# Kernel optimization log

Hardware: AMD Instinct MI355X
Metric: run time of the kernel (lower is better)

## Reference

```python
import jax, jax.numpy as jnp
import numpy as np

N = 16384      # nodes per graph (128x128 image)
E = 9 * N      # 8-neighborhood + self edges
C = 512        # input feature channels
M = 32         # matrixSize


def _p(key, shape, scale=0.05):
    return jax.random.normal(key, shape, dtype=jnp.float32) * scale


def setup_inputs() -> dict:
    key = jax.random.key(0)
    ks = jax.random.split(key, 40)
    inp = {
        "cF": jax.random.normal(ks[0], (N, C), dtype=jnp.float32),
        "sF": jax.random.normal(ks[1], (N, C), dtype=jnp.float32),
        "content_edge_index": jax.random.randint(ks[2], (2, E), 0, N),
        "content_selections": jax.random.randint(ks[3], (E,), 0, 9),
        "style_edge_index": jax.random.randint(ks[4], (2, E), 0, N),
        "style_selections": jax.random.randint(ks[5], (E,), 0, 9),
        "compress_W": _p(ks[6], (1, C, M)),   # kernel_size=1 -> 1 selection
        "compress_b": _p(ks[7], (M,)),
        "unzip_W": _p(ks[8], (1, M, C)),
        "unzip_b": _p(ks[9], (C,)),
    }
    i = 10
    for net in ("cnet", "snet"):
        for j, (ci, co) in enumerate([(C, 256), (256, 128), (128, M)], 1):
            inp[f"{net}_W{j}"] = _p(ks[i], (9, ci, co)); i += 1  # kernel_size=3 -> 9 selections
            inp[f"{net}_b{j}"] = _p(ks[i], (co,)); i += 1
        inp[f"{net}_fcW"] = _p(ks[i], (M * M, M * M)); i += 1   # torch Linear [out,in]
        inp[f"{net}_fcb"] = _p(ks[i], (M * M,)); i += 1
    return inp


def sel_conv(x, edge_index, sel, W, b):
    """SelectionConv: per-selection weight, gather from src, scatter-add to dst.
    x: [N,Cin], W: [S,Cin,Cout]. Edges with selection >= S are masked (kernel_size=1)."""
    S = W.shape[0]
    t = jnp.einsum('nc,scd->snd', x, W)              # [S, N, Cout]
    src, dst = edge_index[0], edge_index[1]
    msgs = t[jnp.minimum(sel, S - 1), src]           # [E, Cout]
    msgs = jnp.where((sel < S)[:, None], msgs, 0.0)
    return jax.ops.segment_sum(msgs, dst, num_segments=x.shape[0]) + b


def cnn_net(x, ei, sel, W1, b1, W2, b2, W3, b3, fcW, fcb):
    h = jax.nn.relu(sel_conv(x, ei, sel, W1, b1))
    h = jax.nn.relu(sel_conv(h, ei, sel, W2, b2))
    h = sel_conv(h, ei, sel, W3, b3)                 # [N, M]
    g = (h.T @ h) / h.shape[0]                       # [M, M] gram
    return g.reshape(-1) @ fcW.T + fcb               # [M*M]


def reference(cF, sF, content_edge_index, content_selections, style_edge_index,
              style_selections, compress_W, compress_b, unzip_W, unzip_b,
              cnet_W1, cnet_b1, cnet_W2, cnet_b2, cnet_W3, cnet_b3, cnet_fcW, cnet_fcb,
              snet_W1, snet_b1, snet_W2, snet_b2, snet_W3, snet_b3, snet_fcW, snet_fcb):
    cMean = jnp.mean(cF, axis=0, keepdims=True)
    cFc = cF - cMean
    sMean = jnp.mean(sF, axis=0, keepdims=True)
    sFc = sF - sMean
    compress_content = sel_conv(cFc, content_edge_index, content_selections,
                                compress_W, compress_b)          # [N, M]
    m = compress_W.shape[2]
    cMat = cnn_net(cFc, content_edge_index, content_selections,
                   cnet_W1, cnet_b1, cnet_W2, cnet_b2, cnet_W3, cnet_b3,
                   cnet_fcW, cnet_fcb).reshape(m, m)
    sMat = cnn_net(sFc, style_edge_index, style_selections,
                   snet_W1, snet_b1, snet_W2, snet_b2, snet_W3, snet_b3,
                   snet_fcW, snet_fcb).reshape(m, m)
    transmatrix = sMat @ cMat                                    # [M, M]
    transfeature = (transmatrix @ compress_content.T).T          # [N, M]
    out = sel_conv(transfeature, content_edge_index, content_selections,
                   unzip_W, unzip_b) + sMean                     # [N, 512]
    return (out, transmatrix)
```

## Files before the change

kernel.cpp:

```cpp
#include <hip/hip_runtime.h>
#include <hip/hip_bf16.h>
#include <cstddef>
#include <cstdint>

#define NN 16384
#define EE (9*NN)
#define CC 512

typedef __attribute__((ext_vector_type(4))) float f32x4;
typedef __attribute__((ext_vector_type(8))) short bf16x8;

static inline int idiv(int a, int b){ return (a+b-1)/b; }

__device__ __forceinline__ float bf2f(unsigned short u){
    union{unsigned u; float f;} v; v.u = ((unsigned)u) << 16; return v.f;
}
__device__ __forceinline__ unsigned short f2bf(float f){
    union{float f; unsigned u;} v; v.f = f;
    unsigned r = v.u + 0x7fffu + ((v.u >> 16) & 1u);
    return (unsigned short)(r >> 16);
}

__device__ __forceinline__ void gload16(const void* gsrc, void* ldst){
    __builtin_amdgcn_global_load_lds(
        (const __attribute__((address_space(1))) unsigned int*)gsrc,
        (__attribute__((address_space(3))) unsigned int*)ldst,
        16, 0, 0);
}


__global__ void zero_i(int* __restrict__ p, int n){
    int i = blockIdx.x*256 + threadIdx.x; if (i < n) p[i] = 0;
}

__global__ void colsum2(const float* __restrict__ F0, float* __restrict__ cs0,
                        const float* __restrict__ F1, float* __restrict__ cs1){
    const float* F = blockIdx.z ? F1 : F0;
    float* cs = blockIdx.z ? cs1 : cs0;
    const int RPB = NN/256;
    int r0 = blockIdx.x * RPB;
    int c4 = threadIdx.x;
    float4 s = {0.f,0.f,0.f,0.f};
    for (int r = 0; r < RPB; ++r){
        float4 v = ((const float4*)(F + (size_t)(r0+r)*CC))[c4];
        s.x += v.x; s.y += v.y; s.z += v.z; s.w += v.w;
    }
    atomicAdd(&cs[c4*4+0], s.x);
    atomicAdd(&cs[c4*4+1], s.y);
    atomicAdd(&cs[c4*4+2], s.z);
    atomicAdd(&cs[c4*4+3], s.w);
}

__global__ void center2(const float* __restrict__ F0, const float* __restrict__ cs0,
                        ushort4* __restrict__ o0,
                        const float* __restrict__ F1, const float* __restrict__ cs1,
                        ushort4* __restrict__ o1){
    const float* F = blockIdx.z ? F1 : F0;
    const float* cs = blockIdx.z ? cs1 : cs0;
    ushort4* o = blockIdx.z ? o1 : o0;
    int i = blockIdx.x*256 + threadIdx.x;
    float4 v = ((const float4*)F)[i];
    int c = (i << 2) & (CC-1);
    float4 m = *(const float4*)(cs + c);
    ushort4 r;
    r.x = f2bf(v.x - m.x*(1.f/NN));
    r.y = f2bf(v.y - m.y*(1.f/NN));
    r.z = f2bf(v.z - m.z*(1.f/NN));
    r.w = f2bf(v.w - m.w*(1.f/NN));
    o[i] = r;
}

__global__ void wtrans(const float* __restrict__ W, unsigned short* __restrict__ Wt,
                       int S, int K, int Cout, int Npad, int Kpad){
    int idx = blockIdx.x*256 + threadIdx.x;
    if (idx >= Npad*Kpad) return;
    int colp = idx / Kpad, k = idx - colp*Kpad;
    int s = colp / Cout, j = colp - s*Cout;
    float v = 0.f;
    if (s < S && k < K) v = W[((size_t)s*K + k)*Cout + j];
    Wt[idx] = f2bf(v);
}

__global__ void wtrans2z(const float* __restrict__ W0, const float* __restrict__ W1,
                         unsigned short* __restrict__ Wt0, unsigned short* __restrict__ Wt1,
                         int K, int Cout){
    __shared__ float tile[32][129];
    int s = blockIdx.z % 9;
    const float* W = (blockIdx.z < 9) ? W0 : W1;
    unsigned short* Wt = (blockIdx.z < 9) ? Wt0 : Wt1;
    int jb = blockIdx.x*128, kb = blockIdx.y*32;
    const float* Ws = W + (size_t)s*K*Cout;
    for (int r = 0; r < 32; ++r)
        tile[r][threadIdx.x] = Ws[(size_t)(kb+r)*Cout + jb + threadIdx.x];
    __syncthreads();
    int kk = threadIdx.x & 31, j0 = threadIdx.x >> 5;
    for (int jj = j0; jj < 128; jj += 4)
        Wt[(size_t)(s*Cout + jb + jj)*K + kb + kk] = f2bf(tile[kk][jj]);
}

__global__ void csr_count3(const int* __restrict__ cDst, const int* __restrict__ sDst,
                           const int* __restrict__ cSel,
                           int* __restrict__ cCnt, int* __restrict__ sCnt, int* __restrict__ cCnt0){
    int e = blockIdx.x*256 + threadIdx.x;
    if (e >= EE) return;
    int z = blockIdx.z;
    if (z == 0)      atomicAdd(&cCnt[cDst[e]], 1);
    else if (z == 1) atomicAdd(&sCnt[sDst[e]], 1);
    else if (cSel[e] == 0) atomicAdd(&cCnt0[cDst[e]], 1);
}
__global__ void csr_scan3(const int* __restrict__ c0, const int* __restrict__ c1,
                          const int* __restrict__ c2,
                          int* __restrict__ r0, int* __restrict__ r1, int* __restrict__ r2){
    const int* cnt = blockIdx.z==0 ? c0 : (blockIdx.z==1 ? c1 : c2);
    int* rowptr    = blockIdx.z==0 ? r0 : (blockIdx.z==1 ? r1 : r2);
    __shared__ int part[1024];
    int t = threadIdx.x;
    int base = t*16, s = 0;
    int local[16];
    #pragma unroll
    for (int i = 0; i < 16; ++i){ local[i] = s; s += cnt[base+i]; }
    part[t] = s; __syncthreads();
    for (int off = 1; off < 1024; off <<= 1){
        int v = (t >= off) ? part[t-off] : 0;
        __syncthreads();
        part[t] += v;
        __syncthreads();
    }
    int pre = (t == 0) ? 0 : part[t-1];
    #pragma unroll
    for (int i = 0; i < 16; ++i) rowptr[base+i] = pre + local[i];
    if (t == 1023) rowptr[NN] = part[1023];
}
__global__ void csr_fill3(const int* __restrict__ cSrc, const int* __restrict__ cDst,
                          const int* __restrict__ cSel,
                          const int* __restrict__ sSrc, const int* __restrict__ sDst,
                          const int* __restrict__ sSel,
                          const int* __restrict__ cRow, const int* __restrict__ sRow,
                          const int* __restrict__ cRow0,
                          int* __restrict__ cCur, int* __restrict__ sCur, int* __restrict__ cCur0,
                          int* __restrict__ cEl, int* __restrict__ sEl, int* __restrict__ cEl0){
    int e = blockIdx.x*256 + threadIdx.x;
    if (e >= EE) return;
    int z = blockIdx.z;
    if (z == 0){
        int d = cDst[e];
        int p = atomicAdd(&cCur[d], 1);
        cEl[cRow[d] + p] = (cSrc[e] << 4) | cSel[e];
    } else if (z == 1){
        int d = sDst[e];
        int p = atomicAdd(&sCur[d], 1);
        sEl[sRow[d] + p] = (sSrc[e] << 4) | sSel[e];
    } else if (cSel[e] == 0){
        int d = cDst[e];
        int p = atomicAdd(&cCur0[d], 1);
        cEl0[cRow0[d] + p] = cSrc[e];
    }
}

template<typename OutT>
__global__ __launch_bounds__(256, 2)
void mfma_gemm(const unsigned short* __restrict__ A0, const unsigned short* __restrict__ Bt0,
               OutT* __restrict__ C0,
               const unsigned short* __restrict__ A1, const unsigned short* __restrict__ Bt1,
               OutT* __restrict__ C1, int K, int N){
    const unsigned short* A  = blockIdx.z ? A1 : A0;
    const unsigned short* Bt = blockIdx.z ? Bt1 : Bt0;
    OutT* C = blockIdx.z ? C1 : C0;
    __shared__ __align__(16) unsigned short As[128*64];
    __shared__ __align__(16) unsigned short Bs[128*64];
    const int tid  = threadIdx.x;
    const int wave = tid >> 6, lane = tid & 63;
    const int row0 = blockIdx.y << 7, col0 = blockIdx.x << 7;
    const int wm = wave >> 1, wn = wave & 1;
    const int fr = lane & 15, fq = lane >> 4;
    f32x4 acc[4][4] = {};
    for (int k0 = 0; k0 < K; k0 += 64){
        __syncthreads();
        #pragma unroll
        for (int i = 0; i < 4; ++i){
            int chb = (wave*4 + i) * 64;
            int ch  = chb + lane;
            int r   = ch >> 3, c8 = ch & 7;
            gload16((const char*)(A  + (size_t)(row0 + r)*K + k0) + c8*16, As + chb*8);
            gload16((const char*)(Bt + (size_t)(col0 + r)*K + k0) + c8*16, Bs + chb*8);
        }
        __syncthreads();
        #pragma unroll
        for (int ks = 0; ks < 2; ++ks){
            bf16x8 av[4], bv[4];
            #pragma unroll
            for (int m = 0; m < 4; ++m)
                av[m] = *(const bf16x8*)(As + ((wm<<6)+(m<<4)+fr)*64 + (ks<<5) + (fq<<3));
            #pragma unroll
            for (int n = 0; n < 4; ++n)
                bv[n] = *(const bf16x8*)(Bs + ((wn<<6)+(n<<4)+fr)*64 + (ks<<5) + (fq<<3));
            #pragma unroll
            for (int m = 0; m < 4; ++m)
                #pragma unroll
                for (int n = 0; n < 4; ++n)
                    acc[m][n] = __builtin_amdgcn_mfma_f32_16x16x32_bf16(bv[n], av[m], acc[m][n], 0, 0, 0);
        }
    }
    #pragma unroll
    for (int m = 0; m < 4; ++m){
        int row = row0 + (wm<<6) + (m<<4) + fr;
        OutT* crow = C + (size_t)row*N + col0 + (wn<<6) + (fq<<2);
        #pragma unroll
        for (int n = 0; n < 4; ++n){
            if constexpr (sizeof(OutT) == 2){
                unsigned lo = f2bf(acc[m][n][0]) | ((unsigned)f2bf(acc[m][n][1]) << 16);
                unsigned hi = f2bf(acc[m][n][2]) | ((unsigned)f2bf(acc[m][n][3]) << 16);
                uint2 pk; pk.x = lo; pk.y = hi;
                *(uint2*)((unsigned short*)crow + (n<<4)) = pk;
            } else {
                float4 pk; pk.x = acc[m][n][0]; pk.y = acc[m][n][1];
                pk.z = acc[m][n][2]; pk.w = acc[m][n][3];
                *(float4*)((float*)crow + (n<<4)) = pk;
            }
        }
    }
}

template<int MQ, int NQ>
__device__ __forceinline__ void mfmaq(f32x4 (&acc)[8][4], bf16x8 (&a)[4][2], bf16x8 (&b)[2][2]){
    #pragma unroll
    for (int m = 0; m < 4; ++m)
        #pragma unroll
        for (int n = 0; n < 2; ++n)
            #pragma unroll
            for (int ks = 0; ks < 2; ++ks)
                acc[MQ*4+m][NQ*2+n] = __builtin_amdgcn_mfma_f32_16x16x32_bf16(
                    b[n][ks], a[m][ks], acc[MQ*4+m][NQ*2+n], 0, 0, 0);
}

#define MIDBAR() do{ __builtin_amdgcn_s_barrier(); \
                     asm volatile("s_waitcnt lgkmcnt(0)" ::: "memory"); \
                     __builtin_amdgcn_sched_barrier(0); \
                     __builtin_amdgcn_s_setprio(1); }while(0)
#define ENDBAR() do{ __builtin_amdgcn_s_setprio(0); \
                     __builtin_amdgcn_s_barrier(); }while(0)

template<int NK>
__global__ __launch_bounds__(512, 1)
void gemm8p(const unsigned short* __restrict__ Ain0, const unsigned short* __restrict__ Btin0,
            unsigned short* __restrict__ Cout0,
            const unsigned short* __restrict__ Ain1, const unsigned short* __restrict__ Btin1,
            unsigned short* __restrict__ Cout1, int N){
    constexpr int LDK = NK*64;
    const unsigned short* A  = blockIdx.z ? Ain1 : Ain0;
    const unsigned short* Bt = blockIdx.z ? Btin1 : Btin0;
    unsigned short* C = blockIdx.z ? Cout1 : Cout0;
    __shared__ __align__(16) unsigned short lds[2][4][8192];
    const int tid = threadIdx.x, w = tid >> 6, l = tid & 63;
    const int nbx = gridDim.x;
    const int nwg = gridDim.x * gridDim.y;
    int blin = blockIdx.y * nbx + blockIdx.x;
    int sw = (blin & 7) * (nwg >> 3) + (blin >> 3);
    const int bx = sw % nbx, by = sw / nbx;
    const int row0 = by << 8, col0 = bx << 8;
    const int wm = w >> 2, wn = w & 3;
    const int fr = l & 15, fq = l >> 4;

    f32x4 acc[8][4] = {};
    bf16x8 a[4][2], b01[2][2], b23[2][2];

    const unsigned short* gA = A + (size_t)row0 * LDK;
    const unsigned short* gB = Bt + (size_t)col0 * LDK;

    auto STG = [&](const unsigned short* gbase, int t, int half, unsigned short* ldsHalf){
        #pragma unroll
        for (int s = 0; s < 2; ++s){
            int o = s*8192 + w*1024 + l*16;
            int q = o ^ ((o >> 3) & 0x70);
            int row = q >> 7;
            gload16((const char*)(gbase + (size_t)(half*128 + row)*LDK + t*64) + (q & 127),
                    ldsHalf + s*4096 + w*512);
        }
    };
    auto LDA = [&](const unsigned short* half, int rb, int ks){
        int lg = (rb*16 + fr)*128 + ks*64 + fq*16;
        int ph = lg ^ ((fr & 7) << 4);
        return *(const bf16x8*)((const char*)half + ph);
    };

    STG(gA, 0, 0, &lds[0][0][0]); STG(gA, 0, 1, &lds[0][1][0]);
    STG(gB, 0, 0, &lds[0][2][0]); STG(gB, 0, 1, &lds[0][3][0]);
    STG(gB, 1, 0, &lds[1][2][0]); STG(gB, 1, 1, &lds[1][3][0]);
    asm volatile("s_waitcnt vmcnt(4)" ::: "memory");
    __builtin_amdgcn_s_barrier();

    const unsigned short* myA[2] = { &lds[0][wm][0], &lds[1][wm][0] };
    const unsigned short* myB[2] = { &lds[0][2+(wn>>1)][0], &lds[1][2+(wn>>1)][0] };
    const int brb = (wn & 1) * 4;

    for (int i = 0; i < NK/2; ++i){
        const int t0 = 2*i, t1 = 2*i + 1;
        #pragma unroll
        for (int m = 0; m < 4; ++m){ a[m][0] = LDA(myA[0], m, 0); a[m][1] = LDA(myA[0], m, 1); }
        #pragma unroll
        for (int n = 0; n < 2; ++n){ b01[n][0] = LDA(myB[0], brb+n, 0); b01[n][1] = LDA(myB[0], brb+n, 1); }
        STG(gA, t1, 0, &lds[1][0][0]);
        MIDBAR(); mfmaq<0,0>(acc, a, b01); ENDBAR();
        #pragma unroll
        for (int n = 0; n < 2; ++n){ b23[n][0] = LDA(myB[0], brb+2+n, 0); b23[n][1] = LDA(myB[0], brb+2+n, 1); }
        STG(gA, t1, 1, &lds[1][1][0]);
        MIDBAR(); mfmaq<0,1>(acc, a, b23); ENDBAR();
        #pragma unroll
        for (int m = 0; m < 4; ++m){ a[m][0] = LDA(myA[0], 4+m, 0); a[m][1] = LDA(myA[0], 4+m, 1); }
        STG(gB, t0+2, 0, &lds[0][2][0]);
        MIDBAR(); mfmaq<1,0>(acc, a, b01); ENDBAR();
        STG(gB, t0+2, 1, &lds[0][3][0]);
        asm volatile("s_waitcnt vmcnt(4)" ::: "memory");
        MIDBAR(); mfmaq<1,1>(acc, a, b23); ENDBAR();
        #pragma unroll
        for (int m = 0; m < 4; ++m){ a[m][0] = LDA(myA[1], m, 0); a[m][1] = LDA(myA[1], m, 1); }
        #pragma unroll
        for (int n = 0; n < 2; ++n){ b01[n][0] = LDA(myB[1], brb+n, 0); b01[n][1] = LDA(myB[1], brb+n, 1); }
        STG(gA, t0+2, 0, &lds[0][0][0]);
        MIDBAR(); mfmaq<0,0>(acc, a, b01); ENDBAR();
        #pragma unroll
        for (int n = 0; n < 2; ++n){ b23[n][0] = LDA(myB[1], brb+2+n, 0); b23[n][1] = LDA(myB[1], brb+2+n, 1); }
        STG(gA, t0+2, 1, &lds[0][1][0]);
        MIDBAR(); mfmaq<0,1>(acc, a, b23); ENDBAR();
        #pragma unroll
        for (int m = 0; m < 4; ++m){ a[m][0] = LDA(myA[1], 4+m, 0); a[m][1] = LDA(myA[1], 4+m, 1); }
        STG(gB, t1+2, 0, &lds[1][2][0]);
        MIDBAR(); mfmaq<1,0>(acc, a, b01); ENDBAR();
        STG(gB, t1+2, 1, &lds[1][3][0]);
        asm volatile("s_waitcnt vmcnt(4)" ::: "memory");
        MIDBAR(); mfmaq<1,1>(acc, a, b23); ENDBAR();
    }
    asm volatile("s_waitcnt vmcnt(0)" ::: "memory");

    #pragma unroll
    for (int m = 0; m < 8; ++m){
        int row = row0 + wm*128 + m*16 + fr;
        unsigned short* crow = C + (size_t)row*N + col0 + wn*64 + fq*4;
        #pragma unroll
        for (int n = 0; n < 4; ++n){
            unsigned lo = f2bf(acc[m][n][0]) | ((unsigned)f2bf(acc[m][n][1]) << 16);
            unsigned hi = f2bf(acc[m][n][2]) | ((unsigned)f2bf(acc[m][n][3]) << 16);
            uint2 pk; pk.x = lo; pk.y = hi;
            *(uint2*)(crow + (n<<4)) = pk;
        }
    }
}

template<typename TO, bool RELU>
__global__ void gather8z(const int* __restrict__ rp0, const int* __restrict__ el0,
                         const unsigned short* __restrict__ t0, const float* __restrict__ b0,
                         TO* __restrict__ o0,
                         const int* __restrict__ rp1, const int* __restrict__ el1,
                         const unsigned short* __restrict__ t1, const float* __restrict__ b1,
                         TO* __restrict__ o1,
                         int tStride, int coutShift){
    const int* rowptr = blockIdx.z ? rp1 : rp0;
    const int* elist  = blockIdx.z ? el1 : el0;
    const unsigned short* t = blockIdx.z ? t1 : t0;
    const float* bias = blockIdx.z ? b1 : b0;
    TO* out = blockIdx.z ? o1 : o0;
    int idx = blockIdx.x*256 + threadIdx.x;
    int chSh = coutShift - 3;
    int d = idx >> chSh;
    int c0 = (idx & ((1 << chSh) - 1)) << 3;
    float acc[8];
    {
        const float4* bb = (const float4*)(bias + c0);
        float4 a = bb[0], b = bb[1];
        acc[0]=a.x; acc[1]=a.y; acc[2]=a.z; acc[3]=a.w;
        acc[4]=b.x; acc[5]=b.y; acc[6]=b.z; acc[7]=b.w;
    }
    int j1 = rowptr[d+1];
    #pragma unroll 2
    for (int j = rowptr[d]; j < j1; ++j){
        int p = elist[j];
        int s = p & 15, sr = p >> 4;
        bf16x8 v = *(const bf16x8*)(t + (size_t)sr*tStride + (s << coutShift) + c0);
        #pragma unroll
        for (int k = 0; k < 8; ++k) acc[k] += bf2f((unsigned short)v[k]);
    }
    if (RELU){
        #pragma unroll
        for (int k = 0; k < 8; ++k) acc[k] = fmaxf(acc[k], 0.f);
    }
    if constexpr (sizeof(TO) == 2){
        union { bf16x8 v; unsigned short u[8]; } r;
        #pragma unroll
        for (int k = 0; k < 8; ++k) r.u[k] = f2bf(acc[k]);
        *(bf16x8*)((unsigned short*)out + ((size_t)d << coutShift) + c0) = r.v;
    } else {
        float4 a = {acc[0],acc[1],acc[2],acc[3]};
        float4 b = {acc[4],acc[5],acc[6],acc[7]};
        float4* op = (float4*)((float*)out + ((size_t)d << coutShift) + c0);
        op[0] = a; op[1] = b;
    }
}

template<bool ADDV>
__global__ void gather4f(const int* __restrict__ rowptr, const int* __restrict__ elist,
                         const float* __restrict__ t,
                         const float* __restrict__ bias, const float* __restrict__ addvec,
                         float* __restrict__ out, int tStride, int coutShift){
    int idx = blockIdx.x*256 + threadIdx.x;
    int chSh = coutShift - 2;
    int d = idx >> chSh;
    int c0 = (idx & ((1 << chSh) - 1)) << 2;
    float4 bb = *(const float4*)(bias + c0);
    float acc0 = bb.x, acc1 = bb.y, acc2 = bb.z, acc3 = bb.w;
    if (ADDV){
        float4 av = *(const float4*)(addvec + c0);
        acc0 += av.x*(1.f/NN); acc1 += av.y*(1.f/NN);
        acc2 += av.z*(1.f/NN); acc3 += av.w*(1.f/NN);
    }
    int j1 = rowptr[d+1];
    #pragma unroll 2
    for (int j = rowptr[d]; j < j1; ++j){
        int sr = elist[j];
        float4 v = *(const float4*)(t + (size_t)sr*tStride + c0);
        acc0 += v.x; acc1 += v.y; acc2 += v.z; acc3 += v.w;
    }
    float4 r = {acc0, acc1, acc2, acc3};
    *(float4*)(out + ((size_t)d << coutShift) + c0) = r;
}

__global__ void gram2(const float* __restrict__ h0, float* __restrict__ g0,
                      const float* __restrict__ h1, float* __restrict__ g1){
    const float* h = blockIdx.z ? h1 : h0;
    float* g = blockIdx.z ? g1 : g0;
    const int RPB = NN/64;
    int r0 = blockIdx.x*RPB;
    int i = threadIdx.x >> 5, j = threadIdx.x & 31;
    float s = 0.f;
    for (int r = 0; r < RPB; ++r){
        const float* row = h + (size_t)(r0+r)*32;
        s += row[i]*row[j];
    }
    atomicAdd(&g[threadIdx.x], s);
}

__global__ void fc2(const float* __restrict__ g0, const float* __restrict__ fcW0,
                    const float* __restrict__ fcb0, float* __restrict__ o0,
                    const float* __restrict__ g1, const float* __restrict__ fcW1,
                    const float* __restrict__ fcb1, float* __restrict__ o1){
    const float* g   = blockIdx.z ? g1 : g0;
    const float* fcW = blockIdx.z ? fcW1 : fcW0;
    const float* fcb = blockIdx.z ? fcb1 : fcb0;
    float* outMat    = blockIdx.z ? o1 : o0;
    int i = blockIdx.x;
    float s = 0.f;
    for (int j = threadIdx.x; j < 1024; j += 256)
        s += g[j] * (1.f/NN) * fcW[(size_t)i*1024 + j];
    __shared__ float red[256];
    red[threadIdx.x] = s; __syncthreads();
    for (int off = 128; off > 0; off >>= 1){
        if (threadIdx.x < off) red[threadIdx.x] += red[threadIdx.x+off];
        __syncthreads();
    }
    if (threadIdx.x == 0) outMat[i] = red[0] + fcb[i];
}

__global__ void mm32_kernel(const float* __restrict__ A, const float* __restrict__ B,
                            float* __restrict__ T){
    int i = threadIdx.x >> 5, j = threadIdx.x & 31;
    float s = 0.f;
    for (int k = 0; k < 32; ++k) s += A[i*32+k]*B[k*32+j];
    T[threadIdx.x] = s;
}

__global__ void tf_cvt_kernel(const float* __restrict__ cc, const float* __restrict__ T,
                              unsigned short* __restrict__ tfbB){
    __shared__ float Ts[1024];
    for (int i = threadIdx.x; i < 1024; i += blockDim.x) Ts[i] = T[i];
    __syncthreads();
    int idx = blockIdx.x*blockDim.x + threadIdx.x;
    int n = idx >> 5, i = idx & 31;
    float s = 0.f;
    const float* crow = cc + (size_t)n*32;
    #pragma unroll
    for (int j = 0; j < 32; ++j) s += crow[j] * Ts[i*32+j];
    tfbB[(size_t)n*64 + i] = f2bf(s);
    tfbB[(size_t)n*64 + 32 + i] = 0;
}

extern "C" void kernel_launch(void* const* d_in, const int* in_sizes, int n_in,
                              void* d_out, int out_size, void* d_ws, size_t ws_size,
                              hipStream_t stream){
    const float* cF   = (const float*)d_in[0];
    const float* sF   = (const float*)d_in[1];
    const int*   cEI  = (const int*)d_in[2];
    const int*   cSel = (const int*)d_in[3];
    const int*   sEI  = (const int*)d_in[4];
    const int*   sSel = (const int*)d_in[5];
    const float* compW= (const float*)d_in[6];
    const float* compB= (const float*)d_in[7];
    const float* unzW = (const float*)d_in[8];
    const float* unzB = (const float*)d_in[9];
    const float* cW1=(const float*)d_in[10]; const float* cB1=(const float*)d_in[11];
    const float* cW2=(const float*)d_in[12]; const float* cB2=(const float*)d_in[13];
    const float* cW3=(const float*)d_in[14]; const float* cB3=(const float*)d_in[15];
    const float* cFW=(const float*)d_in[16]; const float* cFB=(const float*)d_in[17];
    const float* sW1=(const float*)d_in[18]; const float* sB1=(const float*)d_in[19];
    const float* sW2=(const float*)d_in[20]; const float* sB2=(const float*)d_in[21];
    const float* sW3=(const float*)d_in[22]; const float* sB3=(const float*)d_in[23];
    const float* sFW=(const float*)d_in[24]; const float* sFB=(const float*)d_in[25];

    float* out  = (float*)d_out;
    float* Tmat = out + (size_t)NN*CC;

    char* w = (char*)d_ws;
    auto alloc = [&](size_t b)->char*{ char* p = w; w += (b + 255) & ~(size_t)255; return p; };
    float* cCol = (float*)alloc(512*4);
    float* sCol = (float*)alloc(512*4);
    float* cg   = (float*)alloc(1024*4);
    float* sg   = (float*)alloc(1024*4);
    float* cMat = (float*)alloc(1024*4);
    float* sMat = (float*)alloc(1024*4);
    int* cCnt = (int*)alloc(NN*4);
    int* cCur = (int*)alloc(NN*4);
    int* sCnt = (int*)alloc(NN*4);
    int* sCur = (int*)alloc(NN*4);
    int* cCnt0= (int*)alloc(NN*4);
    int* cCur0= (int*)alloc(NN*4);
    int* cRow = (int*)alloc((NN+1)*4);
    int* sRow = (int*)alloc((NN+1)*4);
    int* cRow0= (int*)alloc((NN+1)*4);
    int* cEl  = (int*)alloc(EE*4);
    int* sEl  = (int*)alloc(EE*4);
    int* cEl0 = (int*)alloc(EE*4);
    float* ccbuf = (float*)alloc((size_t)NN*32*4);
    unsigned short* tfbB = (unsigned short*)alloc((size_t)NN*64*2);
    unsigned short* wtC1 = (unsigned short*)alloc((size_t)2304*512*2);
    unsigned short* wtC2 = (unsigned short*)alloc((size_t)1280*256*2);
    unsigned short* wtC3 = (unsigned short*)alloc((size_t)384*128*2);
    unsigned short* wtS1 = (unsigned short*)alloc((size_t)2304*512*2);
    unsigned short* wtS2 = (unsigned short*)alloc((size_t)1280*256*2);
    unsigned short* wtS3 = (unsigned short*)alloc((size_t)384*128*2);
    unsigned short* wtCo = (unsigned short*)alloc((size_t)128*512*2);
    unsigned short* wtU  = (unsigned short*)alloc((size_t)512*64*2);
    unsigned short* cFcB = (unsigned short*)alloc((size_t)NN*512*2);
    unsigned short* sFcB = (unsigned short*)alloc((size_t)NN*512*2);
    float* h3c = (float*)alloc((size_t)NN*32*4);
    float* h3s = (float*)alloc((size_t)NN*32*4);
    unsigned short* tC = (unsigned short*)alloc((size_t)NN*2304*2);
    unsigned short* tS = (unsigned short*)alloc((size_t)NN*2304*2);
    float* tFc = (float*)tC;
    unsigned short* h1c = cFcB;
    unsigned short* h1s = sFcB;
    unsigned short* h2c = cFcB + (size_t)NN*256;
    unsigned short* h2s = sFcB + (size_t)NN*256;

    const int* cSrc = cEI; const int* cDst = cEI + EE;
    const int* sSrc = sEI; const int* sDst = sEI + EE;

    int zeroInts = (int)(((char*)cCur0 - (char*)d_ws)/4) + NN;
    zero_i<<<idiv(zeroInts,256),256,0,stream>>>((int*)d_ws, zeroInts);

    colsum2<<<dim3(256,1,2),128,0,stream>>>(cF, cCol, sF, sCol);
    center2<<<dim3(NN*CC/1024,1,2),256,0,stream>>>(cF, cCol, (ushort4*)cFcB,
                                                   sF, sCol, (ushort4*)sFcB);

    wtrans2z<<<dim3(2,16,18),128,0,stream>>>(cW1, sW1, wtC1, wtS1, 512, 256);
    wtrans2z<<<dim3(1,8,18),128,0,stream>>>(cW2, sW2, wtC2, wtS2, 256, 128);
    wtrans<<<idiv(384*128,256),256,0,stream>>>(cW3, wtC3, 9,128,32, 384,128);
    wtrans<<<idiv(384*128,256),256,0,stream>>>(sW3, wtS3, 9,128,32, 384,128);
    wtrans<<<idiv(128*512,256),256,0,stream>>>(compW, wtCo, 1,512,32, 128,512);
    wtrans<<<idiv(512*64,256),256,0,stream>>>(unzW,  wtU,  1,32,512, 512,64);

    csr_count3<<<dim3(idiv(EE,256),1,3),256,0,stream>>>(cDst, sDst, cSel, cCnt, sCnt, cCnt0);
    csr_scan3<<<dim3(1,1,3),1024,0,stream>>>(cCnt, sCnt, cCnt0, cRow, sRow, cRow0);
    csr_fill3<<<dim3(idiv(EE,256),1,3),256,0,stream>>>(cSrc,cDst,cSel, sSrc,sDst,sSel,
                                                       cRow,sRow,cRow0, cCur,sCur,cCur0,
                                                       cEl,sEl,cEl0);

    mfma_gemm<float><<<dim3(1,128,1),256,0,stream>>>(cFcB, wtCo, tFc, cFcB, wtCo, tFc, 512, 128);
    gather4f<false><<<NN*8/256,256,0,stream>>>(cRow0,cEl0,tFc,compB,nullptr,ccbuf,128,5);

    gemm8p<8><<<dim3(9,64,2),512,0,stream>>>(cFcB, wtC1, tC, sFcB, wtS1, tS, 2304);
    gather8z<unsigned short,true><<<dim3(2048,1,2),256,0,stream>>>(
        cRow,cEl,tC,cB1,h1c, sRow,sEl,tS,sB1,h1s, 2304, 8);
    gemm8p<4><<<dim3(5,64,2),512,0,stream>>>(h1c, wtC2, tC, h1s, wtS2, tS, 1280);
    gather8z<unsigned short,true><<<dim3(1024,1,2),256,0,stream>>>(
        cRow,cEl,tC,cB2,h2c, sRow,sEl,tS,sB2,h2s, 1280, 7);
    mfma_gemm<unsigned short><<<dim3(3,128,2),256,0,stream>>>(h2c, wtC3, tC, h2s, wtS3, tS, 128, 384);
    gather8z<float,false><<<dim3(256,1,2),256,0,stream>>>(
        cRow,cEl,tC,cB3,h3c, sRow,sEl,tS,sB3,h3s, 384, 5);
    gram2<<<dim3(64,1,2),1024,0,stream>>>(h3c, cg, h3s, sg);
    fc2<<<dim3(1024,1,2),256,0,stream>>>(cg,cFW,cFB,cMat, sg,sFW,sFB,sMat);

    mm32_kernel<<<1,1024,0,stream>>>(sMat, cMat, Tmat);
    tf_cvt_kernel<<<NN*32/256,256,0,stream>>>(ccbuf, Tmat, tfbB);

    mfma_gemm<float><<<dim3(4,128,1),256,0,stream>>>(tfbB, wtU, tFc, tfbB, wtU, tFc, 64, 512);
    gather4f<true><<<NN*128/256,256,0,stream>>>(cRow0,cEl0,tFc,unzB,sCol,out,512,9);
}
```

Before: 438.2 us.

## Replace layer-1 GEMM with double-buffered 128x128 tile kernel and merge weight transposes

Adds a new gemm_db kernel that uses 128x128 output tiles, 256 threads, a two-stage LDS double buffer with swizzled addressing and block-index swizzling. It replaces the 256-wide gemm8p<8> for the large first-layer transform (K=512, N=2304). The separate cW3/sW3 weight-transpose launches are merged into one z-batched launch to cut launch count. The smaller tiles raise block count and occupancy, but each tile reuses less data and the kernel uses a simple __syncthreads pipeline in place of the hand-scheduled waits of gemm8p.

```diff
diff --git a/kernel.cpp b/kernel.cpp
--- a/kernel.cpp
+++ b/kernel.cpp
@@ -70,8 +70,11 @@
     o[i] = r;
 }
 
-__global__ void wtrans(const float* __restrict__ W, unsigned short* __restrict__ Wt,
-                       int S, int K, int Cout, int Npad, int Kpad){
+__global__ void wtransz(const float* __restrict__ W0, unsigned short* __restrict__ Wt0,
+                        const float* __restrict__ W1, unsigned short* __restrict__ Wt1,
+                        int S, int K, int Cout, int Npad, int Kpad){
+    const float* W = blockIdx.z ? W1 : W0;
+    unsigned short* Wt = blockIdx.z ? Wt1 : Wt0;
     int idx = blockIdx.x*256 + threadIdx.x;
     if (idx >= Npad*Kpad) return;
     int colp = idx / Kpad, k = idx - colp*Kpad;
@@ -342,6 +345,92 @@
             unsigned hi = f2bf(acc[m][n][2]) | ((unsigned)f2bf(acc[m][n][3]) << 16);
             uint2 pk; pk.x = lo; pk.y = hi;
             *(uint2*)(crow + (n<<4)) = pk;
+        }
+    }
+}
+
+template<int NT, typename OutT>
+__global__ __launch_bounds__(256, 3)
+void gemm_db(const unsigned short* __restrict__ A0, const unsigned short* __restrict__ Bt0,
+             OutT* __restrict__ C0,
+             const unsigned short* __restrict__ A1, const unsigned short* __restrict__ Bt1,
+             OutT* __restrict__ C1, int N){
+    constexpr int LDK = NT*32;
+    const unsigned short* A  = blockIdx.z ? A1 : A0;
+    const unsigned short* Bt = blockIdx.z ? Bt1 : Bt0;
+    OutT* C = blockIdx.z ? C1 : C0;
+    __shared__ __align__(16) unsigned short lds[2][2][4096];
+    const int tid = threadIdx.x, w = tid >> 6, l = tid & 63;
+    const int wm = w >> 1, wn = w & 1;
+    const int fr = l & 15, fq = l >> 4;
+    const int nbx = gridDim.x;
+    const int nwg = gridDim.x * gridDim.y;
+    int blin = blockIdx.y * nbx + blockIdx.x;
+    int sw = (blin & 7) * (nwg >> 3) + (blin >> 3);
+    const int bx = sw % nbx, by = sw / nbx;
+    const int row0 = by << 7, col0 = bx << 7;
+
+    const unsigned short* gA = A + (size_t)row0 * LDK;
+    const unsigned short* gB = Bt + (size_t)col0 * LDK;
+
+    auto STG = [&](int buf, int t){
+        #pragma unroll
+        for (int mtx = 0; mtx < 2; ++mtx){
+            const unsigned short* gb = mtx ? gB : gA;
+            #pragma unroll
+            for (int ld = 0; ld < 2; ++ld){
+                int o = (ld*256 + tid) * 16;
+                int row = o >> 6;
+                int kb = (o & 63) ^ ((row & 3) << 4);
+                gload16((const char*)(gb + (size_t)row*LDK + t*32) + kb,
+                        (char*)&lds[buf][mtx][0] + o);
+            }
+        }
+    };
+
+    f32x4 acc[4][4] = {};
+    STG(0, 0);
+    __syncthreads();
+    for (int t = 0; t < NT; ++t){
+        int cur = t & 1;
+        if (t + 1 < NT) STG(cur ^ 1, t + 1);
+        bf16x8 av[4], bv[4];
+        #pragma unroll
+        for (int m = 0; m < 4; ++m){
+            int r = wm*64 + m*16 + fr;
+            int p = (r*64 + fq*16) ^ ((r & 3) << 4);
+            av[m] = *(const bf16x8*)((const char*)&lds[cur][0][0] + p);
+        }
+        #pragma unroll
+        for (int n = 0; n < 4; ++n){
+            int r = wn*64 + n*16 + fr;
+            int p = (r*64 + fq*16) ^ ((r & 3) << 4);
+            bv[n] = *(const bf16x8*)((const char*)&lds[cur][1][0] + p);
+        }
+        #pragma unroll
+        for (int m = 0; m < 4; ++m)
+            #pragma unroll
+            for (int n = 0; n < 4; ++n)
+                acc[m][n] = __builtin_amdgcn_mfma_f32_16x16x32_bf16(bv[n], av[m], acc[m][n], 0, 0, 0);
+        __syncthreads();
+    }
+
+    #pragma unroll
+    for (int m = 0; m < 4; ++m){
+        int row = row0 + wm*64 + m*16 + fr;
+        OutT* crow = C + (size_t)row*N + col0 + (wn<<6) + (fq<<2);
+        #pragma unroll
+        for (int n = 0; n < 4; ++n){
+            if constexpr (sizeof(OutT) == 2){
+                unsigned lo = f2bf(acc[m][n][0]) | ((unsigned)f2bf(acc[m][n][1]) << 16);
+                unsigned hi = f2bf(acc[m][n][2]) | ((unsigned)f2bf(acc[m][n][3]) << 16);
+                uint2 pk; pk.x = lo; pk.y = hi;
+                *(uint2*)((unsigned short*)crow + (n<<4)) = pk;
+            } else {
+                float4 pk; pk.x = acc[m][n][0]; pk.y = acc[m][n][1];
+                pk.z = acc[m][n][2]; pk.w = acc[m][n][3];
+                *(float4*)((float*)crow + (n<<4)) = pk;
+            }
         }
     }
 }
@@ -561,10 +650,9 @@
 
     wtrans2z<<<dim3(2,16,18),128,0,stream>>>(cW1, sW1, wtC1, wtS1, 512, 256);
     wtrans2z<<<dim3(1,8,18),128,0,stream>>>(cW2, sW2, wtC2, wtS2, 256, 128);
-    wtrans<<<idiv(384*128,256),256,0,stream>>>(cW3, wtC3, 9,128,32, 384,128);
-    wtrans<<<idiv(384*128,256),256,0,stream>>>(sW3, wtS3, 9,128,32, 384,128);
-    wtrans<<<idiv(128*512,256),256,0,stream>>>(compW, wtCo, 1,512,32, 128,512);
-    wtrans<<<idiv(512*64,256),256,0,stream>>>(unzW,  wtU,  1,32,512, 512,64);
+    wtransz<<<dim3(idiv(384*128,256),1,2),256,0,stream>>>(cW3, wtC3, sW3, wtS3, 9,128,32, 384,128);
+    wtransz<<<dim3(idiv(128*512,256),1,1),256,0,stream>>>(compW, wtCo, compW, wtCo, 1,512,32, 128,512);
+    wtransz<<<dim3(idiv(512*64,256),1,1),256,0,stream>>>(unzW, wtU, unzW, wtU, 1,32,512, 512,64);
 
     csr_count3<<<dim3(idiv(EE,256),1,3),256,0,stream>>>(cDst, sDst, cSel, cCnt, sCnt, cCnt0);
     csr_scan3<<<dim3(1,1,3),1024,0,stream>>>(cCnt, sCnt, cCnt0, cRow, sRow, cRow0);
@@ -572,16 +660,19 @@
                                                        cRow,sRow,cRow0, cCur,sCur,cCur0,
                                                        cEl,sEl,cEl0);
 
-    mfma_gemm<float><<<dim3(1,128,1),256,0,stream>>>(cFcB, wtCo, tFc, cFcB, wtCo, tFc, 512, 128);
+    mfma_gemm<float><<<dim3(1,128,1),256,0,stream>>>(cFcB, wtCo, tFc,
+                                                     cFcB, wtCo, tFc, 512, 128);
     gather4f<false><<<NN*8/256,256,0,stream>>>(cRow0,cEl0,tFc,compB,nullptr,ccbuf,128,5);
 
-    gemm8p<8><<<dim3(9,64,2),512,0,stream>>>(cFcB, wtC1, tC, sFcB, wtS1, tS, 2304);
+    gemm_db<16,unsigned short><<<dim3(18,128,2),256,0,stream>>>(cFcB, wtC1, tC,
+                                                                sFcB, wtS1, tS, 2304);
     gather8z<unsigned short,true><<<dim3(2048,1,2),256,0,stream>>>(
         cRow,cEl,tC,cB1,h1c, sRow,sEl,tS,sB1,h1s, 2304, 8);
     gemm8p<4><<<dim3(5,64,2),512,0,stream>>>(h1c, wtC2, tC, h1s, wtS2, tS, 1280);
     gather8z<unsigned short,true><<<dim3(1024,1,2),256,0,stream>>>(
         cRow,cEl,tC,cB2,h2c, sRow,sEl,tS,sB2,h2s, 1280, 7);
-    mfma_gemm<unsigned short><<<dim3(3,128,2),256,0,stream>>>(h2c, wtC3, tC, h2s, wtS3, tS, 128, 384);
+    mfma_gemm<unsigned short><<<dim3(3,128,2),256,0,stream>>>(h2c, wtC3, tC,
+                                                              h2s, wtS3, tS, 128, 384);
     gather8z<float,false><<<dim3(256,1,2),256,0,stream>>>(
         cRow,cEl,tC,cB3,h3c, sRow,sEl,tS,sB3,h3s, 384, 5);
     gram2<<<dim3(64,1,2),1024,0,stream>>>(h3c, cg, h3s, sg);
@@ -590,6 +681,7 @@
     mm32_kernel<<<1,1024,0,stream>>>(sMat, cMat, Tmat);
     tf_cvt_kernel<<<NN*32/256,256,0,stream>>>(ccbuf, Tmat, tfbB);
 
-    mfma_gemm<float><<<dim3(4,128,1),256,0,stream>>>(tfbB, wtU, tFc, tfbB, wtU, tFc, 64, 512);
+    mfma_gemm<float><<<dim3(4,128,1),256,0,stream>>>(tfbB, wtU, tFc,
+                                                     tfbB, wtU, tFc, 64, 512);
     gather4f<true><<<NN*128/256,256,0,stream>>>(cRow0,cEl0,tFc,unzB,sCol,out,512,9);
 }
```

Measured after the change: 420.6 us. 1.04x faster.
